# Optimization experiments

Hardware: AMD Instinct MI355X
Metric: run time of the kernel (lower is better)

## Reference

```python
import jax, jax.numpy as jnp
import numpy as np

N_NODES = 100000
N_EDGES = 1600000
D_IN = 128
D_HID = 128
D_OUT = 10
N_GRAPHS = 512


def _sage_conv(x, src, dst, W_l, b_l, W_r, num_nodes):
    # PyG SAGEConv (mean aggr): out = lin_l(mean_{j in N(i)} x_j) + lin_r(x_i)
    msg = x[src]                                            # [E, D] gather
    s = jax.ops.segment_sum(msg, dst, num_segments=num_nodes)
    cnt = jax.ops.segment_sum(jnp.ones((src.shape[0], 1), x.dtype), dst,
                              num_segments=num_nodes)
    mean = s / jnp.maximum(cnt, 1.0)                        # 0 where no neighbors
    return mean @ W_l.T + b_l + x @ W_r.T


def setup_inputs() -> dict:
    key = jax.random.key(0)
    ks = jax.random.split(key, 10)
    glorot = lambda k, o, i: jax.random.normal(k, (o, i), jnp.float32) * (1.0 / np.sqrt(i))
    return {
        "x": jax.random.normal(ks[0], (N_NODES, D_IN), jnp.float32),
        "edge_index": jax.random.randint(ks[1], (2, N_EDGES), 0, N_NODES, jnp.int64),
        "batch": jnp.sort(jax.random.randint(ks[2], (N_NODES,), 0, N_GRAPHS, jnp.int64)),
        "W1_l": glorot(ks[3], D_HID, D_IN),
        "b1": jnp.zeros((D_HID,), jnp.float32),
        "W1_r": glorot(ks[4], D_HID, D_IN),
        "W2_l": glorot(ks[5], D_HID, D_HID),
        "b2": jnp.zeros((D_HID,), jnp.float32),
        "W2_r": glorot(ks[6], D_HID, D_HID),
        "Wf": glorot(ks[7], D_OUT, D_HID),
        "bf": jnp.zeros((D_OUT,), jnp.float32),
    }


def reference(x, edge_index, batch, W1_l, b1, W1_r, W2_l, b2, W2_r, Wf, bf):
    src, dst = edge_index[0], edge_index[1]
    n = x.shape[0]
    h = jax.nn.relu(_sage_conv(x, src, dst, W1_l, b1, W1_r, n))
    h = jax.nn.relu(_sage_conv(h, src, dst, W2_l, b2, W2_r, n))
    # global_mean_pool over graph ids
    gsum = jax.ops.segment_sum(h, batch, num_segments=N_GRAPHS)
    gcnt = jax.ops.segment_sum(jnp.ones((n, 1), h.dtype), batch, num_segments=N_GRAPHS)
    g = gsum / jnp.maximum(gcnt, 1.0)
    logits = g @ Wf.T + bf
    return jax.nn.log_softmax(logits, axis=-1)
```

## Files before the change

kernel.cpp:

```cpp
#include <hip/hip_runtime.h>
#include <hip/hip_bf16.h>

#define N_NODES 100000
#define N_EDGES 1600000
#define N_GRAPHS 512
#define NB 256
#define NPB 391
#define CHUNK 6250
#define STAGE 7680
#define GGROUPS 1563
#define GGRID 512

typedef __attribute__((ext_vector_type(8))) short short8;
typedef __attribute__((ext_vector_type(4))) float f32x4;
typedef __attribute__((ext_vector_type(2))) float f32x2;

__device__ __forceinline__ float b2f(ushort u) {
    union { unsigned int i; float f; } c; c.i = ((unsigned int)u) << 16; return c.f;
}
__device__ __forceinline__ float blo(unsigned int u) {
    union { unsigned int i; float f; } c; c.i = u << 16; return c.f;
}
__device__ __forceinline__ float bhi(unsigned int u) {
    union { unsigned int i; float f; } c; c.i = u & 0xffff0000u; return c.f;
}
__device__ __forceinline__ ushort f2b(float f) {
    union { float f; unsigned int i; } c; c.f = f;
    unsigned int r = (c.i + 0x7fffu + ((c.i >> 16) & 1u)) >> 16;
    return (ushort)r;
}
__device__ __forceinline__ unsigned int fbits(float f) {
    union { float f; unsigned int i; } c; c.f = f; return c.i;
}
__device__ __forceinline__ int idx_at(const void* p, long i, int f) {
    return f ? (int)((const long long*)p)[i] : ((const int*)p)[i];
}
__device__ __forceinline__ short8 dec8v(uint2 q) {
    f32x2 d0 = __builtin_amdgcn_cvt_pk_f32_fp8((int)q.x, false);
    f32x2 d1 = __builtin_amdgcn_cvt_pk_f32_fp8((int)q.x, true);
    f32x2 d2 = __builtin_amdgcn_cvt_pk_f32_fp8((int)q.y, false);
    f32x2 d3 = __builtin_amdgcn_cvt_pk_f32_fp8((int)q.y, true);
    union { short8 s; unsigned int u[4]; } r;
    r.u[0] = __builtin_amdgcn_perm(fbits(d0.y), fbits(d0.x), 0x07060302u);
    r.u[1] = __builtin_amdgcn_perm(fbits(d1.y), fbits(d1.x), 0x07060302u);
    r.u[2] = __builtin_amdgcn_perm(fbits(d2.y), fbits(d2.x), 0x07060302u);
    r.u[3] = __builtin_amdgcn_perm(fbits(d3.y), fbits(d3.x), 0x07060302u);
    return r.s;
}

__global__ __launch_bounds__(256) void k_detect(const unsigned int* __restrict__ xw,
                                                const unsigned int* __restrict__ ew,
                                                const int* __restrict__ bw,
                                                int* __restrict__ flags) {
    __shared__ int cf, ce, cb;
    int t = threadIdx.x;
    if (t == 0) { cf = 0; ce = 0; cb = 0; }
    __syncthreads();
    unsigned int w = xw[t];
    unsigned int e = (w >> 7) & 0xffu;
    if (e >= 110u && e <= 130u) atomicAdd(&cf, 1);
    if (t < 128) {
        if (ew[2 * t + 1] != 0u) atomicAdd(&ce, 1);
        if (bw[99001 + 2 * t] != 0) atomicAdd(&cb, 1);
    }
    __syncthreads();
    if (t == 0) {
        flags[0] = (cf >= 128) ? 1 : 0;
        flags[1] = (ce == 0) ? 1 : 0;
        flags[2] = (cb == 0) ? 1 : 0;
    }
}

__global__ __launch_bounds__(256) void k_prep(const void* __restrict__ ei,
                                              const void* __restrict__ x,
                                              unsigned int* __restrict__ xf8,
                                              const void* W1l, const void* W1r,
                                              const void* W2l, const void* W2r,
                                              const void* b1,  const void* b2,
                                              ushort* __restrict__ wbf,
                                              int* __restrict__ blkcnt,
                                              float* __restrict__ gsum,
                                              const int* __restrict__ flags) {
    int b = blockIdx.x, t = threadIdx.x;
    if (b < NB) {
        __shared__ int h[NB];
        int f = flags[1];
        for (int j = t; j < NB; j += 256) h[j] = 0;
        __syncthreads();
        int lo = b * CHUNK, hi = lo + CHUNK;
        for (int e = lo + t; e < hi; e += 256) {
            int d = idx_at(ei, (long)N_EDGES + e, f);
            atomicAdd(&h[d / NPB], 1);
        }
        __syncthreads();
        if (t < NB) blkcnt[b * NB + t] = h[t];
    } else if (b < NB + 2048) {
        bool f32src = (flags[0] == 0);
        int vb = b - NB;
        const long nG = (long)N_NODES * 128 / 4;
        for (long g = (long)vb * 256 + t; g < nG; g += 2048L * 256) {
            float v0, v1, v2, v3;
            if (f32src) {
                float4 vv = ((const float4*)x)[g];
                v0 = vv.x; v1 = vv.y; v2 = vv.z; v3 = vv.w;
            } else {
                uint2 q = ((const uint2*)x)[g];
                v0 = blo(q.x); v1 = bhi(q.x); v2 = blo(q.y); v3 = bhi(q.y);
            }
            int r = __builtin_amdgcn_cvt_pk_fp8_f32(v0, v1, 0, false);
            r = __builtin_amdgcn_cvt_pk_fp8_f32(v2, v3, r, true);
            xf8[g] = (unsigned int)r;
        }
    } else if (b < NB + 2048 + 257) {
        int idx = (b - NB - 2048) * 256 + t;
        if (idx >= 65792) return;
        const void* src; int off;
        if      (idx < 16384) { src = W1l; off = idx; }
        else if (idx < 32768) { src = W1r; off = idx - 16384; }
        else if (idx < 49152) { src = W2l; off = idx - 32768; }
        else if (idx < 65536) { src = W2r; off = idx - 49152; }
        else if (idx < 65664) { src = b1;  off = idx - 65536; }
        else                  { src = b2;  off = idx - 65664; }
        wbf[idx] = (flags[0] != 0) ? ((const ushort*)src)[off]
                                   : f2b(((const float*)src)[off]);
    } else {
        int idx = (b - NB - 2048 - 257) * 256 + t;
        gsum[idx] = 0.f;
    }
}

__global__ __launch_bounds__(NB) void k_bscan(const int* __restrict__ blkcnt,
                                              int* __restrict__ bucketBase,
                                              int* __restrict__ blkbase) {
    __shared__ int s[NB];
    int t = threadIdx.x;
    int tot = 0;
    for (int blk = 0; blk < NB; ++blk) tot += blkcnt[blk * NB + t];
    s[t] = tot; __syncthreads();
    for (int off = 1; off < NB; off <<= 1) {
        int a = (t >= off) ? s[t - off] : 0;
        __syncthreads();
        s[t] += a;
        __syncthreads();
    }
    int excl = s[t] - tot;
    bucketBase[t] = excl;
    if (t == NB - 1) bucketBase[NB] = s[NB - 1];
    int run = excl;
    for (int blk = 0; blk < NB; ++blk) {
        blkbase[blk * NB + t] = run;
        run += blkcnt[blk * NB + t];
    }
}

__global__ __launch_bounds__(256) void k_bin(const void* __restrict__ ei,
                                             const int* __restrict__ blkbase,
                                             int* __restrict__ binned,
                                             const int* __restrict__ flags) {
    __shared__ int bb[NB];
    __shared__ int rank[NB];
    int t = threadIdx.x, blk = blockIdx.x;
    int f = flags[1];
    for (int j = t; j < NB; j += 256) { bb[j] = blkbase[blk * NB + j]; rank[j] = 0; }
    __syncthreads();
    int lo = blk * CHUNK, hi = lo + CHUNK;
    for (int e = lo + t; e < hi; e += 256) {
        int s = idx_at(ei, e, f);
        int d = idx_at(ei, (long)N_EDGES + e, f);
        int b = d / NPB;
        int loc = d - b * NPB;
        int r = atomicAdd(&rank[b], 1);
        binned[bb[b] + r] = s | (loc << 20);
    }
}

__global__ __launch_bounds__(256) void k_csr(const int* __restrict__ binned,
                                             const int* __restrict__ bucketBase,
                                             int* __restrict__ rowptr,
                                             int* __restrict__ csr) {
    __shared__ int cnt[400];
    __shared__ int sc[400];
    __shared__ int sh[256];
    __shared__ int stage[STAGE];
    int t = threadIdx.x, b = blockIdx.x;
    int nodeLo = b * NPB;
    int nC = N_NODES - nodeLo; if (nC > NPB) nC = NPB;
    int eBase = bucketBase[b], eEnd = bucketBase[b + 1];

    for (int j = t; j < 400; j += 256) cnt[j] = 0;
    __syncthreads();
    for (int i = eBase + t; i < eEnd; i += 256)
        atomicAdd(&cnt[binned[i] >> 20], 1);
    __syncthreads();
    int base = t * 2;
    int v0 = (base < 400) ? cnt[base] : 0;
    int v1 = (base + 1 < 400) ? cnt[base + 1] : 0;
    int ssum = v0 + v1;
    sh[t] = ssum; __syncthreads();
    for (int off = 1; off < 256; off <<= 1) {
        int a = (t >= off) ? sh[t - off] : 0;
        __syncthreads();
        sh[t] += a;
        __syncthreads();
    }
    int pre = sh[t] - ssum;
    if (base < 400) sc[base] = pre;
    if (base + 1 < 400) sc[base + 1] = pre + v0;
    __syncthreads();
    for (int j = t; j < nC; j += 256) rowptr[nodeLo + j] = eBase + sc[j];
    if (b == NB - 1) {
        if (t == 0) rowptr[N_NODES] = eEnd;
        if (t < 64) csr[N_EDGES + t] = 0;
    }
    for (int j = t; j < 400; j += 256) cnt[j] = 0;
    __syncthreads();
    for (int i = eBase + t; i < eEnd; i += 256) {
        int p = binned[i];
        int loc = p >> 20;
        int pos = sc[loc] + atomicAdd(&cnt[loc], 1);
        int srcn = p & 0xFFFFF;
        if (pos < STAGE) stage[pos] = srcn;
        else csr[eBase + pos] = srcn;
    }
    __syncthreads();
    int eCnt = eEnd - eBase; if (eCnt > STAGE) eCnt = STAGE;
    for (int j = t; j < eCnt; j += 256) csr[eBase + j] = stage[j];
}

__global__ __launch_bounds__(256) void k_agg(const uint4* __restrict__ x8,
                                             const int* __restrict__ rowptr,
                                             const int* __restrict__ csr,
                                             uint4* __restrict__ mout) {
    int wv = blockIdx.x * 4 + (threadIdx.x >> 6);
    int lane = threadIdx.x & 63;
    int li = lane & 7;
    int node = wv * 8 + (lane >> 3);
    int beg = rowptr[node];
    int end = rowptr[node + 1];
    int deg = end - beg;
    f32x2 a2[8] = {};
    int full = deg & ~7;
    int j = 0;
    for (; j < full; j += 8) {
        int vidx = csr[beg + j + li];
        uint4 p[8];
#pragma unroll
        for (int i = 0; i < 8; ++i) {
            int idx = __shfl(vidx, i | (lane & 56));
            p[i] = x8[(long)idx * 8 + li];
        }
#pragma unroll
        for (int i = 0; i < 8; ++i) {
            a2[0] += __builtin_amdgcn_cvt_pk_f32_fp8((int)p[i].x, false);
            a2[1] += __builtin_amdgcn_cvt_pk_f32_fp8((int)p[i].x, true);
            a2[2] += __builtin_amdgcn_cvt_pk_f32_fp8((int)p[i].y, false);
            a2[3] += __builtin_amdgcn_cvt_pk_f32_fp8((int)p[i].y, true);
            a2[4] += __builtin_amdgcn_cvt_pk_f32_fp8((int)p[i].z, false);
            a2[5] += __builtin_amdgcn_cvt_pk_f32_fp8((int)p[i].z, true);
            a2[6] += __builtin_amdgcn_cvt_pk_f32_fp8((int)p[i].w, false);
            a2[7] += __builtin_amdgcn_cvt_pk_f32_fp8((int)p[i].w, true);
        }
    }
    if (j < deg) {
        int pos = beg + j + li;
        if (pos > end - 1) pos = end - 1;
        int vidx = csr[pos];
#pragma unroll
        for (int i = 0; i < 8; ++i) {
            int idx = __shfl(vidx, i | (lane & 56));
            uint4 p = x8[(long)idx * 8 + li];
            bool ok = (j + i < deg);
            unsigned int q0 = ok ? p.x : 0u;
            unsigned int q1 = ok ? p.y : 0u;
            unsigned int q2 = ok ? p.z : 0u;
            unsigned int q3 = ok ? p.w : 0u;
            a2[0] += __builtin_amdgcn_cvt_pk_f32_fp8((int)q0, false);
            a2[1] += __builtin_amdgcn_cvt_pk_f32_fp8((int)q0, true);
            a2[2] += __builtin_amdgcn_cvt_pk_f32_fp8((int)q1, false);
            a2[3] += __builtin_amdgcn_cvt_pk_f32_fp8((int)q1, true);
            a2[4] += __builtin_amdgcn_cvt_pk_f32_fp8((int)q2, false);
            a2[5] += __builtin_amdgcn_cvt_pk_f32_fp8((int)q2, true);
            a2[6] += __builtin_amdgcn_cvt_pk_f32_fp8((int)q3, false);
            a2[7] += __builtin_amdgcn_cvt_pk_f32_fp8((int)q3, true);
        }
    }
    float s = (deg > 0) ? 1.f / (float)deg : 0.f;
    uint4 o;
    int r;
    r = __builtin_amdgcn_cvt_pk_fp8_f32(a2[0].x * s, a2[0].y * s, 0, false);
    r = __builtin_amdgcn_cvt_pk_fp8_f32(a2[1].x * s, a2[1].y * s, r, true);  o.x = (unsigned int)r;
    r = __builtin_amdgcn_cvt_pk_fp8_f32(a2[2].x * s, a2[2].y * s, 0, false);
    r = __builtin_amdgcn_cvt_pk_fp8_f32(a2[3].x * s, a2[3].y * s, r, true);  o.y = (unsigned int)r;
    r = __builtin_amdgcn_cvt_pk_fp8_f32(a2[4].x * s, a2[4].y * s, 0, false);
    r = __builtin_amdgcn_cvt_pk_fp8_f32(a2[5].x * s, a2[5].y * s, r, true);  o.z = (unsigned int)r;
    r = __builtin_amdgcn_cvt_pk_fp8_f32(a2[6].x * s, a2[6].y * s, 0, false);
    r = __builtin_amdgcn_cvt_pk_fp8_f32(a2[7].x * s, a2[7].y * s, r, true);  o.w = (unsigned int)r;
    mout[(long)node * 8 + li] = o;
}

__global__ __launch_bounds__(256) void k_gemm(const uchar* __restrict__ A0f8,
                                              const uchar* __restrict__ A1f8,
                                              const ushort* __restrict__ Wl,
                                              const ushort* __restrict__ Wr,
                                              const ushort* __restrict__ bias,
                                              uchar* __restrict__ out8,
                                              float* __restrict__ gsum,
                                              const void* __restrict__ batch,
                                              const int* __restrict__ flags,
                                              int layer1) {
    __shared__ short Ws[4096 * 8];
    __shared__ uint4 Ast4[1024];
    uchar* Ast = (uchar*)Ast4;
    int t = threadIdx.x;
    int wid = t >> 6, lane = t & 63;

    int g0 = blockIdx.x;
    uint4 sreg[4];
#pragma unroll
    for (int c = 0; c < 4; ++c) {
        int cid = c * 256 + t;
        int r = (cid >> 3) & 63, lc8 = cid & 7;
        long grow = (long)g0 * 64 + r; if (grow >= N_NODES) grow = N_NODES - 1;
        const uchar* bp = (cid & 512) ? A1f8 : A0f8;
        sreg[c] = *(const uint4*)(bp + grow * 128 + lc8 * 16);
    }

#pragma unroll
    for (int i = 0; i < 16; ++i) {
        int f = i * 256 + t;
        int ln = f & 63, kk = (f >> 6) & 7, tile = f >> 9;
        int o = tile * 16 + (ln & 15);
        int k0 = kk * 32 + ((ln >> 4) * 8);
        const ushort* wsrc = (k0 < 128) ? (Wl + o * 128 + k0)
                                        : (Wr + o * 128 + (k0 - 128));
        *(short8*)&Ws[f * 8] = *(const short8*)wsrc;
    }
#pragma unroll
    for (int c = 0; c < 4; ++c) {
        int cid = c * 256 + t;
        int buf = cid >> 9, r = (cid >> 3) & 63, lc8 = cid & 7;
        int sc = (buf * 8 + lc8) ^ (r & 15);
        *(uint4*)&Ast[r * 256 + sc * 16] = sreg[c];
    }
    __syncthreads();

    int kq = (lane >> 4) * 8;
    int lm = lane & 15, qh = (lane >> 5) & 1, ql8 = ((lane >> 4) & 1) * 8;
    int rloc = wid * 16 + lm;
    int bflag = layer1 ? 0 : flags[2];
    (void)kq;

    for (int g = g0; g < GGROUPS; g += GGRID) {
        long nbase = (long)g * 64 + (long)wid * 16;

        uint2 raw[8];
        {
            int rb = rloc * 256 + ql8;
#pragma unroll
            for (int kk = 0; kk < 8; ++kk) {
                int sc = ((kk * 2 + qh) ^ lm) << 4;
                raw[kk] = *(const uint2*)&Ast[rb + sc];
            }
        }
        __syncthreads();

        int bg[4]; int guni = 0; bool uniform = false;
        if (!layer1) {
            int bmin = 0x7fffffff, bmax = -0x7fffffff;
#pragma unroll
            for (int r = 0; r < 4; ++r) {
                long node = nbase + (lane >> 4) * 4 + r;
                if (node < N_NODES) {
                    int bb = idx_at(batch, node, bflag);
                    bg[r] = bb;
                    bmin = min(bmin, bb); bmax = max(bmax, bb);
                } else { bg[r] = 0; bmax = 0x7fffffff; }
            }
            bmin = min(bmin, __shfl_xor(bmin, 16));
            bmin = min(bmin, __shfl_xor(bmin, 32));
            bmax = max(bmax, __shfl_xor(bmax, 16));
            bmax = max(bmax, __shfl_xor(bmax, 32));
            uniform = (bmin == bmax);
            guni = bmin;
        }

        int gn = g + GGRID;
        bool havenext = (gn < GGROUPS);
        if (havenext) {
#pragma unroll
            for (int c = 0; c < 4; ++c) {
                int cid = c * 256 + t;
                int r = (cid >> 3) & 63, lc8 = cid & 7;
                long grow = (long)gn * 64 + r; if (grow >= N_NODES) grow = N_NODES - 1;
                const uchar* bp = (cid & 512) ? A1f8 : A0f8;
                sreg[c] = *(const uint4*)(bp + grow * 128 + lc8 * 16);
            }
        }

        short8 afrag[8];
#pragma unroll
        for (int kk = 0; kk < 8; ++kk) afrag[kk] = dec8v(raw[kk]);

#pragma unroll
        for (int tile = 0; tile < 8; ++tile) {
            f32x4 acc = {0.f, 0.f, 0.f, 0.f};
#pragma unroll
            for (int kk = 0; kk < 8; ++kk) {
                short8 bfrag = *(short8*)&Ws[((tile * 8 + kk) * 64 + lane) * 8];
                acc = __builtin_amdgcn_mfma_f32_16x16x32_bf16(afrag[kk], bfrag, acc, 0, 0, 0);
            }
            int o = tile * 16 + (lane & 15);
            float bo = b2f(bias[o]);
            if (layer1) {
#pragma unroll
                for (int r = 0; r < 4; ++r) {
                    long node = nbase + (lane >> 4) * 4 + r;
                    if (node < N_NODES) {
                        float v = acc[r] + bo;
                        v = v > 0.f ? v : 0.f;
                        int pp = __builtin_amdgcn_cvt_pk_fp8_f32(v, v, 0, false);
                        out8[node * 128 + o] = (uchar)pp;
                    }
                }
            } else if (uniform) {
                float s = 0.f;
#pragma unroll
                for (int r = 0; r < 4; ++r) {
                    float v = acc[r] + bo;
                    s += (v > 0.f ? v : 0.f);
                }
                s += __shfl_xor(s, 16);
                s += __shfl_xor(s, 32);
                if ((lane >> 4) == 0) atomicAdd(&gsum[guni * 128 + o], s);
            } else {
#pragma unroll
                for (int r = 0; r < 4; ++r) {
                    long node = nbase + (lane >> 4) * 4 + r;
                    if (node < N_NODES) {
                        float v = acc[r] + bo;
                        v = v > 0.f ? v : 0.f;
                        atomicAdd(&gsum[bg[r] * 128 + o], v);
                    }
                }
            }
        }

        if (havenext) {
#pragma unroll
            for (int c = 0; c < 4; ++c) {
                int cid = c * 256 + t;
                int buf = cid >> 9, r = (cid >> 3) & 63, lc8 = cid & 7;
                int sc = (buf * 8 + lc8) ^ (r & 15);
                *(uint4*)&Ast[r * 256 + sc * 16] = sreg[c];
            }
        }
        __syncthreads();
    }
}

__global__ __launch_bounds__(128) void k_cls(const float* __restrict__ gsum,
                                             const void* __restrict__ batch,
                                             const void* __restrict__ Wf,
                                             const void* __restrict__ bfv,
                                             void* __restrict__ outp,
                                             const int* __restrict__ flags) {
    int g = blockIdx.x, t = threadIdx.x;
    bool f32 = (flags[0] == 0);
    int b64 = flags[2];
    __shared__ int rng[2];
    __shared__ float gv[128];
    __shared__ float lg[10];
    if (t < 2) {
        int v = g + t, lo = 0, hi = N_NODES;
        while (lo < hi) {
            int mid = (lo + hi) >> 1;
            if (idx_at(batch, mid, b64) < v) lo = mid + 1; else hi = mid;
        }
        rng[t] = lo;
    }
    __syncthreads();
    int cnt = rng[1] - rng[0];
    float c = (cnt > 0) ? (float)cnt : 1.f;
    gv[t] = gsum[g * 128 + t] / c;
    __syncthreads();
    if (t < 10) {
        float s = f32 ? ((const float*)bfv)[t] : b2f(((const ushort*)bfv)[t]);
        for (int k = 0; k < 128; ++k) {
            float wv = f32 ? ((const float*)Wf)[t * 128 + k] : b2f(((const ushort*)Wf)[t * 128 + k]);
            s += gv[k] * wv;
        }
        lg[t] = s;
    }
    __syncthreads();
    if (t == 0) {
        float mx = lg[0];
        for (int i = 1; i < 10; ++i) mx = fmaxf(mx, lg[i]);
        float se = 0.f;
        for (int i = 0; i < 10; ++i) se += expf(lg[i] - mx);
        float lse = mx + logf(se);
        for (int i = 0; i < 10; ++i) {
            float v = lg[i] - lse;
            if (f32) ((float*)outp)[g * 10 + i] = v;
            else     ((ushort*)outp)[g * 10 + i] = f2b(v);
        }
    }
}

extern "C" void kernel_launch(void* const* d_in, const int* in_sizes, int n_in,
                              void* d_out, int out_size, void* d_ws, size_t ws_size,
                              hipStream_t stream) {
    const void* x     = d_in[0];
    const void* ei    = d_in[1];
    const void* batch = d_in[2];
    const void* W1l = d_in[3];
    const void* b1  = d_in[4];
    const void* W1r = d_in[5];
    const void* W2l = d_in[6];
    const void* b2  = d_in[7];
    const void* W2r = d_in[8];
    const void* Wf  = d_in[9];
    const void* bf_ = d_in[10];

    char* w = (char*)d_ws;
    int* flags      = (int*)(w + 0);
    int* rowptr     = (int*)(w + 640);
    ushort* wbf     = (ushort*)(w + 400768);
    int* csr        = (int*)(w + 532480);
    float* gsum     = (float*)(w + 6933248);
    uchar* mbuf     = (uchar*)(w + 32533248);
    int* bucketBase = (int*)(w + 32533248);
    int* blkcnt     = (int*)(w + 32534528);
    int* blkbase    = (int*)(w + 32796672);
    uchar* h1f8     = (uchar*)(w + 58133248);
    int* binned     = (int*)(w + 58133248);
    unsigned int* xf8 = (unsigned int*)(w + 70933248);

    dim3 blk256(256), blkNB(NB), blk128(128);

    k_detect<<<1, blk256, 0, stream>>>((const unsigned int*)x, (const unsigned int*)ei,
                                       (const int*)batch, flags);
    k_prep<<<NB + 2048 + 257 + 256, blk256, 0, stream>>>(ei, x, xf8,
                                                         W1l, W1r, W2l, W2r, b1, b2,
                                                         wbf, blkcnt, gsum, flags);
    k_bscan<<<1, blkNB, 0, stream>>>(blkcnt, bucketBase, blkbase);
    k_bin<<<NB, blk256, 0, stream>>>(ei, blkbase, binned, flags);
    k_csr<<<NB, blk256, 0, stream>>>(binned, bucketBase, rowptr, csr);

    int agrid = N_NODES / 8 / 4;

    k_agg<<<agrid, blk256, 0, stream>>>((const uint4*)xf8, rowptr, csr, (uint4*)mbuf);
    k_gemm<<<GGRID, blk256, 0, stream>>>(mbuf, (const uchar*)xf8,
                                         wbf + 0, wbf + 16384, wbf + 65536,
                                         h1f8, (float*)nullptr, nullptr, flags, 1);
    k_agg<<<agrid, blk256, 0, stream>>>((const uint4*)h1f8, rowptr, csr, (uint4*)mbuf);
    k_gemm<<<GGRID, blk256, 0, stream>>>(mbuf, h1f8,
                                         wbf + 32768, wbf + 49152, wbf + 65664,
                                         (uchar*)nullptr, gsum, batch, flags, 0);
    k_cls<<<N_GRAPHS, blk128, 0, stream>>>(gsum, batch, Wf, bf_, d_out, flags);
}
```

Before: 297.7 us.

## Swap MFMA operands to get node-major output and stage fp8 stores through LDS

Swaps the MFMA A/B operands so each lane holds four consecutive output features of one node instead of four nodes of one feature. In layer 1 this lets the fp8 results be packed four per word and staged through a swizzled LDS tile, then written to global memory as coalesced 16-byte rows instead of scattered single-byte stores. For layer 2 the batch-id lookup becomes one load per lane with a 16-lane shuffle reduction, and the bias is read as a vector. The cost is two extra block barriers per group in layer 1, plus LDS reuse of the staging buffer that must not race with the prefetch writes.

```diff
diff --git a/kernel.cpp b/kernel.cpp
--- a/kernel.cpp
+++ b/kernel.cpp
@@ -344,11 +344,10 @@
     }
     __syncthreads();
 
-    int kq = (lane >> 4) * 8;
-    int lm = lane & 15, qh = (lane >> 5) & 1, ql8 = ((lane >> 4) & 1) * 8;
+    int lm = lane & 15, q = lane >> 4;
+    int qh = (lane >> 5) & 1, ql8 = ((lane >> 4) & 1) * 8;
     int rloc = wid * 16 + lm;
     int bflag = layer1 ? 0 : flags[2];
-    (void)kq;
 
     for (int g = g0; g < GGROUPS; g += GGRID) {
         long nbase = (long)g * 64 + (long)wid * 16;
@@ -364,22 +363,18 @@
         }
         __syncthreads();
 
-        int bg[4]; int guni = 0; bool uniform = false;
+        int ndl = (int)nbase + lm;
+        int bgl = 0, guni = 0; bool uniform = false;
         if (!layer1) {
-            int bmin = 0x7fffffff, bmax = -0x7fffffff;
-#pragma unroll
-            for (int r = 0; r < 4; ++r) {
-                long node = nbase + (lane >> 4) * 4 + r;
-                if (node < N_NODES) {
-                    int bb = idx_at(batch, node, bflag);
-                    bg[r] = bb;
-                    bmin = min(bmin, bb); bmax = max(bmax, bb);
-                } else { bg[r] = 0; bmax = 0x7fffffff; }
-            }
-            bmin = min(bmin, __shfl_xor(bmin, 16));
-            bmin = min(bmin, __shfl_xor(bmin, 32));
-            bmax = max(bmax, __shfl_xor(bmax, 16));
-            bmax = max(bmax, __shfl_xor(bmax, 32));
+            bool okn = (ndl < N_NODES);
+            bgl = okn ? idx_at(batch, ndl, bflag) : 0;
+            int bmin = okn ? bgl : 0x7fffffff;
+            int bmax = okn ? bgl : (int)0x80000000;
+#pragma unroll
+            for (int m = 1; m <= 8; m <<= 1) {
+                bmin = min(bmin, __shfl_xor(bmin, m));
+                bmax = max(bmax, __shfl_xor(bmax, m));
+            }
             uniform = (bmin == bmax);
             guni = bmin;
         }
@@ -406,43 +401,60 @@
             f32x4 acc = {0.f, 0.f, 0.f, 0.f};
 #pragma unroll
             for (int kk = 0; kk < 8; ++kk) {
-                short8 bfrag = *(short8*)&Ws[((tile * 8 + kk) * 64 + lane) * 8];
-                acc = __builtin_amdgcn_mfma_f32_16x16x32_bf16(afrag[kk], bfrag, acc, 0, 0, 0);
-            }
-            int o = tile * 16 + (lane & 15);
-            float bo = b2f(bias[o]);
+                short8 wfrag = *(short8*)&Ws[((tile * 8 + kk) * 64 + lane) * 8];
+                acc = __builtin_amdgcn_mfma_f32_16x16x32_bf16(wfrag, afrag[kk], acc, 0, 0, 0);
+            }
+            int o0 = tile * 16 + q * 4;
+            uint2 br = *(const uint2*)(bias + o0);
+            float v0 = acc[0] + blo(br.x);
+            float v1 = acc[1] + bhi(br.x);
+            float v2 = acc[2] + blo(br.y);
+            float v3 = acc[3] + bhi(br.y);
+            v0 = v0 > 0.f ? v0 : 0.f;
+            v1 = v1 > 0.f ? v1 : 0.f;
+            v2 = v2 > 0.f ? v2 : 0.f;
+            v3 = v3 > 0.f ? v3 : 0.f;
             if (layer1) {
-#pragma unroll
-                for (int r = 0; r < 4; ++r) {
-                    long node = nbase + (lane >> 4) * 4 + r;
-                    if (node < N_NODES) {
-                        float v = acc[r] + bo;
-                        v = v > 0.f ? v : 0.f;
-                        int pp = __builtin_amdgcn_cvt_pk_fp8_f32(v, v, 0, false);
-                        out8[node * 128 + o] = (uchar)pp;
-                    }
+                int pp = __builtin_amdgcn_cvt_pk_fp8_f32(v0, v1, 0, false);
+                pp = __builtin_amdgcn_cvt_pk_fp8_f32(v2, v3, pp, true);
+                int nl = wid * 16 + lm;
+                *(unsigned int*)&Ast[nl * 128 + (o0 ^ ((nl & 7) << 4))] = (unsigned int)pp;
+            } else if (uniform) {
+#pragma unroll
+                for (int m = 1; m <= 8; m <<= 1) {
+                    v0 += __shfl_xor(v0, m);
+                    v1 += __shfl_xor(v1, m);
+                    v2 += __shfl_xor(v2, m);
+                    v3 += __shfl_xor(v3, m);
                 }
-            } else if (uniform) {
-                float s = 0.f;
-#pragma unroll
-                for (int r = 0; r < 4; ++r) {
-                    float v = acc[r] + bo;
-                    s += (v > 0.f ? v : 0.f);
+                if (lm == 0) {
+                    atomicAdd(&gsum[guni * 128 + o0 + 0], v0);
+                    atomicAdd(&gsum[guni * 128 + o0 + 1], v1);
+                    atomicAdd(&gsum[guni * 128 + o0 + 2], v2);
+                    atomicAdd(&gsum[guni * 128 + o0 + 3], v3);
                 }
-                s += __shfl_xor(s, 16);
-                s += __shfl_xor(s, 32);
-                if ((lane >> 4) == 0) atomicAdd(&gsum[guni * 128 + o], s);
             } else {
-#pragma unroll
-                for (int r = 0; r < 4; ++r) {
-                    long node = nbase + (lane >> 4) * 4 + r;
-                    if (node < N_NODES) {
-                        float v = acc[r] + bo;
-                        v = v > 0.f ? v : 0.f;
-                        atomicAdd(&gsum[bg[r] * 128 + o], v);
-                    }
+                if (ndl < N_NODES) {
+                    atomicAdd(&gsum[bgl * 128 + o0 + 0], v0);
+                    atomicAdd(&gsum[bgl * 128 + o0 + 1], v1);
+                    atomicAdd(&gsum[bgl * 128 + o0 + 2], v2);
+                    atomicAdd(&gsum[bgl * 128 + o0 + 3], v3);
                 }
             }
+        }
+
+        if (layer1) {
+            __syncthreads();
+#pragma unroll
+            for (int k2 = 0; k2 < 2; ++k2) {
+                int cid = k2 * 256 + t;
+                int row = cid >> 3, c16 = cid & 7;
+                long grow = (long)g * 64 + row;
+                uint4 vq = *(const uint4*)&Ast[row * 128 + ((c16 * 16) ^ ((row & 7) << 4))];
+                if (grow < N_NODES)
+                    *(uint4*)(out8 + grow * 128 + c16 * 16) = vq;
+            }
+            __syncthreads();
         }
 
         if (havenext) {
```

Result: slower. 381.9 us (+28.3%).
